# Kernel tuning notes

Hardware: AMD Instinct MI355X
Metric: run time of the kernel (lower is better)

Reference implementation:

```python
import jax, jax.numpy as jnp
import numpy as np

GROUPS = 32
EPS = 1e-5

def setup_inputs() -> dict:
    key = jax.random.key(0)
    k1, k2, k3 = jax.random.split(key, 3)
    C = 512
    x = jax.random.normal(k1, (4, C, 64, 64), dtype=jnp.float32)
    gn_weight = jnp.ones((C,), jnp.float32)
    gn_bias = jnp.zeros((C,), jnp.float32)
    qkv_weight = jax.random.normal(k2, (3 * C, C), jnp.float32) * (1.0 / np.sqrt(C))
    proj_weight = jax.random.normal(k3, (C, C), jnp.float32) * (1.0 / np.sqrt(C))
    proj_bias = jnp.zeros((C,), jnp.float32)
    return {"x": x, "gn_weight": gn_weight, "gn_bias": gn_bias,
            "qkv_weight": qkv_weight, "proj_weight": proj_weight, "proj_bias": proj_bias}

def reference(x, gn_weight, gn_bias, qkv_weight, proj_weight, proj_bias):
    n, c, h, w = x.shape
    residue = x
    # GroupNorm(32, c): normalize over (c//32 channels * h * w) per group
    xg = x.reshape(n, GROUPS, -1)
    mu = xg.mean(axis=-1, keepdims=True)
    var = xg.var(axis=-1, keepdims=True)
    xn = (xg - mu) * jax.lax.rsqrt(var + EPS)
    xn = xn.reshape(n, c, h, w) * gn_weight[None, :, None, None] + gn_bias[None, :, None, None]
    # tokens: [n, T, c] with T = h*w
    t = xn.reshape(n, c, h * w).transpose(0, 2, 1)
    # qkv linear (no bias), n_heads = 1 so head_size = c
    qkv = jnp.einsum('ntc,dc->ntd', t, qkv_weight)
    q, k, v = jnp.split(qkv, 3, axis=-1)
    scale = 1.0 / np.sqrt(c)
    scores = jnp.einsum('nqc,nkc->nqk', q, k) * scale  # [n, T, T]
    weights = jax.nn.softmax(scores, axis=-1)
    out = jnp.einsum('nqk,nkc->nqc', weights, v)
    out = jnp.einsum('ntc,dc->ntd', out, proj_weight) + proj_bias
    out = out.transpose(0, 2, 1).reshape(n, c, h, w)
    return out + residue
```

## Files before the change

kernel.cpp:

```cpp
#include <hip/hip_runtime.h>
#include <hip/hip_bf16.h>

typedef __bf16 bf16;
typedef __bf16 bf16x8 __attribute__((ext_vector_type(8)));
typedef float f32x4 __attribute__((ext_vector_type(4)));

__device__ __forceinline__ void gload_lds16(const bf16* g, bf16* l) {
    __builtin_amdgcn_global_load_lds(
        (const __attribute__((address_space(1))) void*)g,
        (__attribute__((address_space(3))) void*)l, 16, 0, 0);
}

__global__ __launch_bounds__(256) void k_gnstats(const float* __restrict__ x,
                                                 float2* __restrict__ stats) {
    const int g = blockIdx.x;
    const float4* p = (const float4*)(x + (long)g * 65536);
    float s = 0.f, ss = 0.f;
    #pragma unroll 8
    for (int i = 0; i < 64; ++i) {
        float4 v = p[threadIdx.x + i * 256];
        s  += v.x + v.y + v.z + v.w;
        ss += v.x * v.x + v.y * v.y + v.z * v.z + v.w * v.w;
    }
    #pragma unroll
    for (int off = 32; off >= 1; off >>= 1) {
        s  += __shfl_down(s, off);
        ss += __shfl_down(ss, off);
    }
    __shared__ float rs[4], rss[4];
    if ((threadIdx.x & 63) == 0) { rs[threadIdx.x >> 6] = s; rss[threadIdx.x >> 6] = ss; }
    __syncthreads();
    if (threadIdx.x == 0) {
        float S  = rs[0] + rs[1] + rs[2] + rs[3];
        float SS = rss[0] + rss[1] + rss[2] + rss[3];
        float mu = S * (1.f / 65536.f);
        float var = SS * (1.f / 65536.f) - mu * mu;
        stats[g] = make_float2(mu, rsqrtf(var + 1e-5f));
    }
}

__global__ __launch_bounds__(256) void k_norm_t(const float* __restrict__ x,
                                                const float* __restrict__ w,
                                                const float* __restrict__ b,
                                                const float2* __restrict__ stats,
                                                bf16* __restrict__ t) {
    __shared__ float tile[64][65];
    const int bid = blockIdx.x;
    const int n = bid >> 9, rem = bid & 511;
    const int s0 = (rem >> 3) * 64, c0 = (rem & 7) * 64;
    const int tid = threadIdx.x;
    const int sl = tid & 63, cq = tid >> 6;
    #pragma unroll
    for (int i = 0; i < 16; ++i) {
        const int cl = cq * 16 + i;
        const int c = c0 + cl;
        const float2 st = stats[n * 32 + (c >> 4)];
        const float v = x[((long)(n * 512 + c)) * 4096 + s0 + sl];
        tile[cl][sl] = (v - st.x) * st.y * w[c] + b[c];
    }
    __syncthreads();
    #pragma unroll
    for (int i = 0; i < 16; ++i) {
        const int sl2 = cq * 16 + i;
        const int cl2 = tid & 63;
        t[((long)(n * 4096 + s0 + sl2)) * 512 + c0 + cl2] = (bf16)tile[cl2][sl2];
    }
}

__global__ __launch_bounds__(256) void k_convw(const float* __restrict__ qw,
                                               const float* __restrict__ pw,
                                               bf16* __restrict__ qwb,
                                               bf16* __restrict__ pwb) {
    const int i = blockIdx.x * 256 + threadIdx.x;
    if (i < 786432) {
        float v = qw[i];
        if (i < 512 * 512) v *= 0.06376281516217733f;
        qwb[i] = (bf16)v;
    } else {
        const int j = i - 786432;
        pwb[j] = (bf16)pw[j];
    }
}

__global__ __launch_bounds__(256) void k_vt(const bf16* __restrict__ vbuf,
                                            bf16* __restrict__ Vt) {
    __shared__ bf16 tile[64][66];
    const int bid = blockIdx.x;
    const int n = bid >> 9, rem = bid & 511;
    const int s0 = (rem >> 3) * 64, d0 = (rem & 7) * 64;
    const int tid = threadIdx.x;
    #pragma unroll
    for (int i = 0; i < 16; ++i) {
        const int sl = (tid >> 6) * 16 + i;
        const int dl = tid & 63;
        tile[sl][dl] = vbuf[((long)(n * 4096 + s0 + sl)) * 512 + d0 + dl];
    }
    __syncthreads();
    #pragma unroll
    for (int i = 0; i < 16; ++i) {
        const int dl = (tid >> 6) * 16 + i;
        const int sl = tid & 63;
        Vt[((long)(n * 512 + d0 + dl)) * 4096 + s0 + sl] = tile[sl][dl];
    }
}

#define PH(mh, kk, S_, WN)                                                         \
  {                                                                                \
    if ((mh) == 0) {                                                               \
      _Pragma("unroll")                                                            \
      for (int n = 0; n < 4; ++n) {                                                \
        int row = wn * 64 + n * 16 + lr;                                           \
        int cg = lg ^ ((row >> 1) & 3);                                            \
        bfr[n] = *(const bf16x8*)(BsT + (kk) * 8192 + row * 32 + cg * 8);          \
      }                                                                            \
    }                                                                              \
    _Pragma("unroll")                                                              \
    for (int i = 0; i < 4; ++i) {                                                  \
      int row = wm * 128 + ((mh) * 4 + i) * 16 + lr;                               \
      int cg = lg ^ ((row >> 1) & 3);                                              \
      af[i] = *(const bf16x8*)(AsT + (kk) * 8192 + row * 32 + cg * 8);             \
    }                                                                              \
    if ((S_) >= 0) issue_unit(S_);                                                 \
    __builtin_amdgcn_s_barrier();                                                  \
    asm volatile("" ::: "memory");                                                 \
    __builtin_amdgcn_s_setprio(1);                                                 \
    _Pragma("unroll")                                                              \
    for (int i = 0; i < 4; ++i)                                                    \
      _Pragma("unroll")                                                            \
      for (int n = 0; n < 4; ++n)                                                  \
        acc[(mh) * 4 + i][n] =                                                     \
            __builtin_amdgcn_mfma_f32_16x16x32_bf16(af[i], bfr[n],                 \
                                                    acc[(mh) * 4 + i][n], 0, 0, 0);\
    __builtin_amdgcn_s_setprio(0);                                                 \
    if constexpr ((WN) >= 0)                                                       \
      asm volatile("s_waitcnt vmcnt(%0)" ::"i"(WN) : "memory");                    \
    __builtin_amdgcn_s_barrier();                                                  \
    asm volatile("" ::: "memory");                                                 \
  }

template <int EPI>
__global__ __launch_bounds__(512, 2) void gemm256(
    const bf16* __restrict__ A, int lda, long aZ,
    const bf16* __restrict__ B, int ldb, long bZ,
    bf16* __restrict__ C, int ldc, long cZ, int K,
    bf16* __restrict__ vbuf) {
    __shared__ bf16 As[2 * 2 * 256 * 32];
    __shared__ bf16 Bs[2 * 2 * 256 * 32];
    const int t = threadIdx.x;
    const int wid = t >> 6, l = t & 63;
    const int wm = wid >> 2, wn = wid & 3;
    const int lr = l & 15;
    const int lg = l >> 4;
    const long z = blockIdx.z;

    const int gx = gridDim.x;
    int nwg = gx * gridDim.y;
    int flat = blockIdx.y * gx + blockIdx.x;
    if ((nwg & 7) == 0) { int qq = nwg >> 3; flat = (flat & 7) * qq + (flat >> 3); }
    const int bx = flat % gx, by = flat / gx;

    const bf16* Ab = A + z * aZ + (long)bx * 256 * lda;
    const bf16* Bb = B + z * bZ + (long)by * 256 * ldb;

    const int NT = K >> 6;
    const int NT4 = NT << 2;

    f32x4 acc[8][4];
    #pragma unroll
    for (int i = 0; i < 8; ++i)
        #pragma unroll
        for (int n = 0; n < 4; ++n) acc[i][n] = f32x4{0.f, 0.f, 0.f, 0.f};

    const int srow = t >> 2;
    const int scg0 = t & 3;

    auto issue_unit = [&](int s) {
        int ti = s >> 2, idx = s & 3;
        int kh = idx >> 1, isB = idx & 1;
        const bf16* g = isB ? Bb : Ab;
        int ld = isB ? ldb : lda;
        bf16* lp = (isB ? Bs : As) + ((ti & 1) * 2 + kh) * 8192;
        int k0 = ti * 64 + kh * 32;
        #pragma unroll
        for (int j = 0; j < 2; ++j) {
            int row = j * 128 + srow;
            int cg = scg0 ^ ((row >> 1) & 3);
            gload_lds16(g + (long)row * ld + k0 + cg * 8, lp + (j * 512 + t) * 8);
        }
    };

    #pragma unroll
    for (int s = 0; s < 6; ++s) issue_unit(s);
    asm volatile("s_waitcnt vmcnt(8)" ::: "memory");
    __builtin_amdgcn_s_barrier();
    asm volatile("" ::: "memory");

    bf16x8 bfr[4], af[4];

    for (int ti = 0; ti < NT - 2; ++ti) {
        const bf16* AsT = As + (ti & 1) * 16384;
        const bf16* BsT = Bs + (ti & 1) * 16384;
        const int sb = 4 * ti + 6;
        PH(0, 0, sb + 0, -1)
        PH(1, 0, sb + 1, 8)
        PH(0, 1, sb + 2, -1)
        PH(1, 1, sb + 3, 8)
    }
    {
        const bf16* AsT = As + ((NT - 2) & 1) * 16384;
        const bf16* BsT = Bs + ((NT - 2) & 1) * 16384;
        PH(0, 0, NT4 - 2, -1)
        PH(1, 0, NT4 - 1, 8)
        PH(0, 1, -1, -1)
        PH(1, 1, -1, 4)
    }
    {
        const bf16* AsT = As + ((NT - 1) & 1) * 16384;
        const bf16* BsT = Bs + ((NT - 1) & 1) * 16384;
        PH(0, 0, -1, -1)
        PH(1, 0, -1, 0)
        PH(0, 1, -1, -1)
        PH(1, 1, -1, -1)
    }

    const int row0 = bx * 256 + wm * 128;
    const int col0 = by * 256 + wn * 64;
    const int rq = lg * 4;

    if (EPI == 1) {
        bf16* Cz = C + z * cZ;
        #pragma unroll
        for (int i = 0; i < 8; ++i)
            #pragma unroll
            for (int n = 0; n < 4; ++n) {
                const int col = col0 + n * 16 + lr;
                #pragma unroll
                for (int r = 0; r < 4; ++r)
                    Cz[(long)(row0 + i * 16 + rq + r) * ldc + col] = (bf16)exp2f(acc[i][n][r]);
            }
    } else {
        #pragma unroll
        for (int i = 0; i < 8; ++i) {
            const int row = row0 + i * 16 + rq;
            #pragma unroll
            for (int n = 0; n < 4; ++n) {
                const int col = col0 + n * 16 + lr;
                if (col < 1024) {
                    #pragma unroll
                    for (int r = 0; r < 4; ++r)
                        C[(long)(row + r) * 1024 + col] = (bf16)acc[i][n][r];
                } else {
                    #pragma unroll
                    for (int r = 0; r < 4; ++r)
                        vbuf[(long)(row + r) * 512 + (col - 1024)] = (bf16)acc[i][n][r];
                }
            }
        }
    }
}

__global__ __launch_bounds__(512, 1) void k_pv(
    const bf16* __restrict__ P, const bf16* __restrict__ Vt,
    bf16* __restrict__ O, int ldo) {
    __shared__ bf16 Bs[2][512 * 64];
    __shared__ bf16 As[2][64 * 64];
    __shared__ float linv[64];
    const int t = threadIdx.x;
    const int w = t >> 6, l = t & 63, lr = l & 15, lg = l >> 4;
    const int lr7 = lr & 7;
    const int sr = t >> 3, sc8 = t & 7, sr7 = sr & 7;
    const long zz = blockIdx.y;
    const int bx = blockIdx.x;

    const bf16* Pg = P + zz * ((long)4096 * 4096) + (long)(bx * 64 + sr) * 4096 + (sc8 ^ sr7) * 8;
    const bf16* Vg = Vt + zz * ((long)512 * 4096) + (long)sr * 4096 + (sc8 ^ sr7) * 8;

    auto issue = [&](int tile, int buf) {
        gload_lds16(Pg + tile * 64, As[buf] + t * 8);
        #pragma unroll
        for (int u = 0; u < 8; ++u)
            gload_lds16(Vg + (long)u * 64 * 4096 + tile * 64, Bs[buf] + u * 4096 + t * 8);
    };

    f32x4 acc[4][4];
    #pragma unroll
    for (int i = 0; i < 4; ++i)
        #pragma unroll
        for (int n = 0; n < 4; ++n) acc[i][n] = f32x4{0.f, 0.f, 0.f, 0.f};

    float lsum = 0.f;

    issue(0, 0);
    issue(1, 1);

    for (int ti = 0; ti < 64; ++ti) {
        if (ti < 63) { asm volatile("s_waitcnt vmcnt(9)" ::: "memory"); }
        else         { asm volatile("s_waitcnt vmcnt(0)" ::: "memory"); }
        __builtin_amdgcn_s_barrier();
        asm volatile("" ::: "memory");

        const bf16* Asb = As[ti & 1];
        const bf16* Bsb = Bs[ti & 1];

        {
            bf16x8 sv = *(const bf16x8*)(Asb + t * 8);
            #pragma unroll
            for (int j = 0; j < 8; ++j) lsum += (float)sv[j];
        }

        __builtin_amdgcn_s_setprio(1);
        #pragma unroll
        for (int kk = 0; kk < 2; ++kk) {
            bf16x8 af[4], bfv[4];
            #pragma unroll
            for (int mi = 0; mi < 4; ++mi)
                af[mi] = *(const bf16x8*)(Asb + (mi * 16 + lr) * 64 + (((kk * 4 + lg) ^ lr7) * 8));
            #pragma unroll
            for (int n = 0; n < 4; ++n)
                bfv[n] = *(const bf16x8*)(Bsb + (w * 64 + n * 16 + lr) * 64 + (((kk * 4 + lg) ^ lr7) * 8));
            #pragma unroll
            for (int mi = 0; mi < 4; ++mi)
                #pragma unroll
                for (int n = 0; n < 4; ++n)
                    acc[mi][n] = __builtin_amdgcn_mfma_f32_16x16x32_bf16(af[mi], bfv[n], acc[mi][n], 0, 0, 0);
        }
        __builtin_amdgcn_s_setprio(0);

        __builtin_amdgcn_s_barrier();
        asm volatile("" ::: "memory");
        if (ti < 62) issue(ti + 2, ti & 1);
    }

    lsum += __shfl_xor(lsum, 1);
    lsum += __shfl_xor(lsum, 2);
    lsum += __shfl_xor(lsum, 4);
    if (sc8 == 0) linv[sr] = 1.f / lsum;
    asm volatile("s_waitcnt lgkmcnt(0)" ::: "memory");
    __builtin_amdgcn_s_barrier();
    asm volatile("" ::: "memory");

    bf16* Oz = O + zz * ((long)4096 * ldo);
    #pragma unroll
    for (int mi = 0; mi < 4; ++mi) {
        float4 lv = *(const float4*)&linv[mi * 16 + lg * 4];
        #pragma unroll
        for (int n = 0; n < 4; ++n) {
            const long base = (long)(bx * 64 + mi * 16 + lg * 4) * ldo + w * 64 + n * 16 + lr;
            Oz[base]           = (bf16)(acc[mi][n][0] * lv.x);
            Oz[base + ldo]     = (bf16)(acc[mi][n][1] * lv.y);
            Oz[base + 2 * ldo] = (bf16)(acc[mi][n][2] * lv.z);
            Oz[base + 3 * ldo] = (bf16)(acc[mi][n][3] * lv.w);
        }
    }
}

#define PH128(nh, kk, S_, WN)                                                      \
  {                                                                                \
    if ((nh) == 0) {                                                               \
      _Pragma("unroll")                                                            \
      for (int i = 0; i < 4; ++i) {                                                \
        int row = wm * 64 + i * 16 + lr;                                           \
        int cg = lg ^ ((row >> 1) & 3);                                            \
        af[i] = *(const bf16x8*)(AsT + (kk) * 8192 + row * 32 + cg * 8);           \
      }                                                                            \
    }                                                                              \
    _Pragma("unroll")                                                              \
    for (int j = 0; j < 2; ++j) {                                                  \
      int row = wn * 64 + ((nh) * 2 + j) * 16 + lr;                                \
      int cg = lg ^ ((row >> 1) & 3);                                              \
      bfr[j] = *(const bf16x8*)(BsT + (kk) * 4096 + row * 32 + cg * 8);            \
    }                                                                              \
    if ((S_) >= 0) issue_unit(S_);                                                 \
    __builtin_amdgcn_s_barrier();                                                  \
    asm volatile("" ::: "memory");                                                 \
    __builtin_amdgcn_s_setprio(1);                                                 \
    _Pragma("unroll")                                                              \
    for (int i = 0; i < 4; ++i)                                                    \
      _Pragma("unroll")                                                            \
      for (int j = 0; j < 2; ++j)                                                  \
        acc[i][(nh) * 2 + j] =                                                     \
            __builtin_amdgcn_mfma_f32_16x16x32_bf16(af[i], bfr[j],                 \
                                                    acc[i][(nh) * 2 + j], 0, 0, 0);\
    __builtin_amdgcn_s_setprio(0);                                                 \
    if constexpr ((WN) >= 0)                                                       \
      asm volatile("s_waitcnt vmcnt(%0)" ::"i"(WN) : "memory");                    \
    __builtin_amdgcn_s_barrier();                                                  \
    asm volatile("" ::: "memory");                                                 \
  }

__global__ __launch_bounds__(512, 2) void gemm_proj(
    const bf16* __restrict__ A, int lda,
    const bf16* __restrict__ B, int ldb,
    const float* __restrict__ bias,
    float* __restrict__ Cout) {
    __shared__ bf16 As[2 * 2 * 256 * 32];
    __shared__ bf16 Bs[2 * 2 * 128 * 32];
    const int t = threadIdx.x;
    const int wid = t >> 6, l = t & 63;
    const int wm = wid >> 1, wn = wid & 1;
    const int lr = l & 15;
    const int lg = l >> 4;

    const int gx = gridDim.x;
    int nwg = gx * gridDim.y;
    int flat = blockIdx.y * gx + blockIdx.x;
    if ((nwg & 7) == 0) { int qq = nwg >> 3; flat = (flat & 7) * qq + (flat >> 3); }
    const int bx = flat % gx, by = flat / gx;

    const bf16* Ab = A + (long)bx * 256 * lda;
    const bf16* Bb = B + (long)by * 128 * ldb;

    const int NT = 8;
    const int NT4 = 32;

    f32x4 acc[4][4];
    #pragma unroll
    for (int i = 0; i < 4; ++i)
        #pragma unroll
        for (int n = 0; n < 4; ++n) acc[i][n] = f32x4{0.f, 0.f, 0.f, 0.f};

    const int srow = t >> 2;
    const int scg0 = t & 3;

    auto issue_unit = [&](int s) {
        int ti = s >> 2, idx = s & 3;
        int kh = idx >> 1, isB = idx & 1;
        int k0 = ti * 64 + kh * 32;
        if (isB) {
            bf16* lp = Bs + ((ti & 1) * 2 + kh) * 4096;
            int cg = scg0 ^ ((srow >> 1) & 3);
            gload_lds16(Bb + (long)srow * ldb + k0 + cg * 8, lp + t * 8);
        } else {
            bf16* lp = As + ((ti & 1) * 2 + kh) * 8192;
            #pragma unroll
            for (int j = 0; j < 2; ++j) {
                int row = j * 128 + srow;
                int cg = scg0 ^ ((row >> 1) & 3);
                gload_lds16(Ab + (long)row * lda + k0 + cg * 8, lp + (j * 512 + t) * 8);
            }
        }
    };

    #pragma unroll
    for (int s = 0; s < 6; ++s) issue_unit(s);
    asm volatile("s_waitcnt vmcnt(6)" ::: "memory");
    __builtin_amdgcn_s_barrier();
    asm volatile("" ::: "memory");

    bf16x8 bfr[2], af[4];

    for (int ti = 0; ti < NT - 2; ++ti) {
        const bf16* AsT = As + (ti & 1) * 16384;
        const bf16* BsT = Bs + (ti & 1) * 8192;
        const int sb = 4 * ti + 6;
        PH128(0, 0, sb + 0, -1)
        PH128(1, 0, sb + 1, 6)
        PH128(0, 1, sb + 2, -1)
        PH128(1, 1, sb + 3, 6)
    }
    {
        const bf16* AsT = As + ((NT - 2) & 1) * 16384;
        const bf16* BsT = Bs + ((NT - 2) & 1) * 8192;
        PH128(0, 0, NT4 - 2, -1)
        PH128(1, 0, NT4 - 1, 6)
        PH128(0, 1, -1, -1)
        PH128(1, 1, -1, 3)
    }
    {
        const bf16* AsT = As + ((NT - 1) & 1) * 16384;
        const bf16* BsT = Bs + ((NT - 1) & 1) * 8192;
        PH128(0, 0, -1, -1)
        PH128(1, 0, -1, 0)
        PH128(0, 1, -1, -1)
        PH128(1, 1, -1, -1)
    }

    const int row0 = bx * 256 + wm * 64;
    const int col0 = by * 128 + wn * 64;
    const int rq = lg * 4;
    #pragma unroll
    for (int i = 0; i < 4; ++i)
        #pragma unroll
        for (int n = 0; n < 4; ++n) {
            const int col = col0 + n * 16 + lr;
            #pragma unroll
            for (int r = 0; r < 4; ++r)
                Cout[(long)(row0 + i * 16 + rq + r) * 512 + col] = acc[i][n][r] + bias[col];
        }
}

__global__ __launch_bounds__(256) void k_final(const float* __restrict__ pb,
                                               const float* __restrict__ x,
                                               float* __restrict__ out) {
    __shared__ float tile[64][65];
    const int bid = blockIdx.x;
    const int n = bid >> 9, rem = bid & 511;
    const int s0 = (rem >> 3) * 64, c0 = (rem & 7) * 64;
    const int tid = threadIdx.x;
    #pragma unroll
    for (int i = 0; i < 16; ++i) {
        const int sl = (tid >> 6) * 16 + i;
        const int cl = tid & 63;
        tile[sl][cl] = pb[((long)(n * 4096 + s0 + sl)) * 512 + c0 + cl];
    }
    __syncthreads();
    #pragma unroll
    for (int i = 0; i < 16; ++i) {
        const int cl = (tid >> 6) * 16 + i;
        const int sl = tid & 63;
        const long oi = ((long)(n * 512 + c0 + cl)) * 4096 + s0 + sl;
        out[oi] = tile[sl][cl] + x[oi];
    }
}

extern "C" void kernel_launch(void* const* d_in, const int* in_sizes, int n_in,
                              void* d_out, int out_size, void* d_ws, size_t ws_size,
                              hipStream_t stream) {
    const float* x     = (const float*)d_in[0];
    const float* gnw   = (const float*)d_in[1];
    const float* gnb   = (const float*)d_in[2];
    const float* qkvw  = (const float*)d_in[3];
    const float* projw = (const float*)d_in[4];
    const float* projb = (const float*)d_in[5];

    char* ws = (char*)d_ws;
    size_t off = 0;
    auto alloc = [&](size_t bytes) {
        void* p = ws + off;
        off += (bytes + 255) & ~(size_t)255;
        return p;
    };
    bf16*   qwb   = (bf16*)alloc((size_t)1536 * 512 * 2);
    bf16*   pwb   = (bf16*)alloc((size_t)512 * 512 * 2);
    float2* stats = (float2*)alloc((size_t)128 * 8);
    bf16*   qk    = (bf16*)alloc((size_t)16384 * 1024 * 2);
    bf16*   Vt    = (bf16*)alloc((size_t)4 * 512 * 4096 * 2);
    char*   R     = (char*)alloc((size_t)4 * 4096 * 4096 * 2);
    bf16*   tbuf  = (bf16*)R;
    bf16*   vbuf  = (bf16*)(R + (size_t)16384 * 512 * 2);
    bf16*   Sbuf  = (bf16*)R;
    float*  pjout = (float*)R;

    k_gnstats<<<128, 256, 0, stream>>>(x, stats);
    k_norm_t<<<2048, 256, 0, stream>>>(x, gnw, gnb, stats, tbuf);
    k_convw<<<4096, 256, 0, stream>>>(qkvw, projw, qwb, pwb);

    gemm256<2><<<dim3(64, 6, 1), 512, 0, stream>>>(
        tbuf, 512, 0, qwb, 512, 0, qk, 1024, 0, 512, vbuf);

    k_vt<<<2048, 256, 0, stream>>>(vbuf, Vt);

    const long QZ = (long)4096 * 1024;
    const long SZ = (long)4096 * 4096;
    gemm256<1><<<dim3(16, 16, 4), 512, 0, stream>>>(
        qk, 1024, QZ,
        qk + 512, 1024, QZ,
        Sbuf, 4096, SZ, 512, nullptr);
    k_pv<<<dim3(64, 4), 512, 0, stream>>>(Sbuf, Vt, qk, 1024);

    gemm_proj<<<dim3(64, 4), 512, 0, stream>>>(
        qk, 1024, pwb, 512, projb, pjout);

    k_final<<<2048, 256, 0, stream>>>(pjout, x, (float*)d_out);
}
```

Before: 304.6 us.

## Halve PV k-tile to fit two blocks per CU and remap blocks to XCDs

The P·V kernel now uses a K-tile of 32 instead of 64, halving LDS use so two 512-thread blocks can share a CU (launch bounds raised to 2). The LDS swizzle and load mapping are rewritten for 32-wide rows. The block index is remapped so each XCD handles a contiguous batch of rows of one batch element, which should improve L2 reuse of Vt. The trade-offs are twice as many barrier iterations with less MFMA work per sync, and tighter register limits from the occupancy bound.

```diff
diff --git a/kernel.cpp b/kernel.cpp
--- a/kernel.cpp
+++ b/kernel.cpp
@@ -259,27 +259,39 @@
     }
 }
 
-__global__ __launch_bounds__(512, 1) void k_pv(
+__global__ __launch_bounds__(512, 2) void k_pv(
     const bf16* __restrict__ P, const bf16* __restrict__ Vt,
     bf16* __restrict__ O, int ldo) {
-    __shared__ bf16 Bs[2][512 * 64];
-    __shared__ bf16 As[2][64 * 64];
+    __shared__ bf16 Bs[2][512 * 32];
+    __shared__ bf16 As[2][64 * 32];
     __shared__ float linv[64];
     const int t = threadIdx.x;
     const int w = t >> 6, l = t & 63, lr = l & 15, lg = l >> 4;
-    const int lr7 = lr & 7;
-    const int sr = t >> 3, sc8 = t & 7, sr7 = sr & 7;
-    const long zz = blockIdx.y;
-    const int bx = blockIdx.x;
-
-    const bf16* Pg = P + zz * ((long)4096 * 4096) + (long)(bx * 64 + sr) * 4096 + (sc8 ^ sr7) * 8;
-    const bf16* Vg = Vt + zz * ((long)512 * 4096) + (long)sr * 4096 + (sc8 ^ sr7) * 8;
-
-    auto issue = [&](int tile, int buf) {
-        gload_lds16(Pg + tile * 64, As[buf] + t * 8);
-        #pragma unroll
-        for (int u = 0; u < 8; ++u)
-            gload_lds16(Vg + (long)u * 64 * 4096 + tile * 64, Bs[buf] + u * 4096 + t * 8);
+    const int cgr = lg ^ ((lr >> 1) & 3);
+
+    int f = blockIdx.y * 64 + blockIdx.x;
+    const int xcd = f & 7, idx = f >> 3;
+    const long zz = xcd >> 1;
+    const int bx = (xcd & 1) * 32 + idx;
+
+    const int vr = t >> 2;
+    const int vg = (t & 3) ^ ((vr >> 1) & 3);
+    const bf16* Vgp = Vt + zz * ((long)512 * 4096) + (long)vr * 4096 + vg * 8;
+    const int q = w & 3;
+    const int prl = l >> 2;
+    const int pg = (l & 3) ^ ((l >> 3) & 3);
+    const bf16* Pgp = P + zz * ((long)4096 * 4096)
+                        + (long)(bx * 64 + q * 16 + prl) * 4096 + pg * 8;
+
+    bf16* Asl = &As[0][0];
+    bf16* Bsl = &Bs[0][0];
+
+    auto issue = [&](int ti, int buf) {
+        gload_lds16(Pgp + ti * 32, Asl + buf * 2048 + q * 512 + l * 8);
+        #pragma unroll
+        for (int u = 0; u < 4; ++u)
+            gload_lds16(Vgp + (long)u * 128 * 4096 + ti * 32,
+                        Bsl + buf * 16384 + u * 4096 + t * 8);
     };
 
     f32x4 acc[4][4];
@@ -293,48 +305,46 @@
     issue(0, 0);
     issue(1, 1);
 
-    for (int ti = 0; ti < 64; ++ti) {
-        if (ti < 63) { asm volatile("s_waitcnt vmcnt(9)" ::: "memory"); }
-        else         { asm volatile("s_waitcnt vmcnt(0)" ::: "memory"); }
+    for (int ti = 0; ti < 128; ++ti) {
+        if (ti < 127) { asm volatile("s_waitcnt vmcnt(5)" ::: "memory"); }
+        else          { asm volatile("s_waitcnt vmcnt(0)" ::: "memory"); }
         __builtin_amdgcn_s_barrier();
         asm volatile("" ::: "memory");
 
-        const bf16* Asb = As[ti & 1];
-        const bf16* Bsb = Bs[ti & 1];
-
-        {
-            bf16x8 sv = *(const bf16x8*)(Asb + t * 8);
+        const bf16* Asb = Asl + (ti & 1) * 2048;
+        const bf16* Bsb = Bsl + (ti & 1) * 16384;
+
+        if (w < 4) {
+            bf16x8 sv = *(const bf16x8*)(Asb + q * 512 + l * 8);
             #pragma unroll
             for (int j = 0; j < 8; ++j) lsum += (float)sv[j];
         }
 
         __builtin_amdgcn_s_setprio(1);
-        #pragma unroll
-        for (int kk = 0; kk < 2; ++kk) {
-            bf16x8 af[4], bfv[4];
-            #pragma unroll
-            for (int mi = 0; mi < 4; ++mi)
-                af[mi] = *(const bf16x8*)(Asb + (mi * 16 + lr) * 64 + (((kk * 4 + lg) ^ lr7) * 8));
+        bf16x8 af[4], bfv[4];
+        #pragma unroll
+        for (int mi = 0; mi < 4; ++mi)
+            af[mi] = *(const bf16x8*)(Asb + (mi * 16 + lr) * 32 + cgr * 8);
+        #pragma unroll
+        for (int n = 0; n < 4; ++n)
+            bfv[n] = *(const bf16x8*)(Bsb + (w * 64 + n * 16 + lr) * 32 + cgr * 8);
+        #pragma unroll
+        for (int mi = 0; mi < 4; ++mi)
             #pragma unroll
             for (int n = 0; n < 4; ++n)
-                bfv[n] = *(const bf16x8*)(Bsb + (w * 64 + n * 16 + lr) * 64 + (((kk * 4 + lg) ^ lr7) * 8));
-            #pragma unroll
-            for (int mi = 0; mi < 4; ++mi)
-                #pragma unroll
-                for (int n = 0; n < 4; ++n)
-                    acc[mi][n] = __builtin_amdgcn_mfma_f32_16x16x32_bf16(af[mi], bfv[n], acc[mi][n], 0, 0, 0);
-        }
+                acc[mi][n] = __builtin_amdgcn_mfma_f32_16x16x32_bf16(af[mi], bfv[n], acc[mi][n], 0, 0, 0);
         __builtin_amdgcn_s_setprio(0);
 
         __builtin_amdgcn_s_barrier();
         asm volatile("" ::: "memory");
-        if (ti < 62) issue(ti + 2, ti & 1);
-    }
-
-    lsum += __shfl_xor(lsum, 1);
-    lsum += __shfl_xor(lsum, 2);
-    lsum += __shfl_xor(lsum, 4);
-    if (sc8 == 0) linv[sr] = 1.f / lsum;
+        if (ti < 126) issue(ti + 2, ti & 1);
+    }
+
+    if (w < 4) {
+        lsum += __shfl_xor(lsum, 1);
+        lsum += __shfl_xor(lsum, 2);
+        if ((l & 3) == 0) linv[q * 16 + prl] = 1.f / lsum;
+    }
     asm volatile("s_waitcnt lgkmcnt(0)" ::: "memory");
     __builtin_amdgcn_s_barrier();
     asm volatile("" ::: "memory");
```

New measurement: 335.3 us. 1.1x slower.

## Make GEMM blocks persistent over multiple output tiles with continuous prefetch

Applied to the files above, without the earlier changes.

The templated GEMM now makes each workgroup compute several output tiles in sequence: two column tiles for the QKV projection, and all four batch slices for the QK^T score GEMM. The global-to-LDS prefetch pipeline runs across tile boundaries, so the next tile's loads overlap the current tile's epilogue stores. This is meant to remove pipeline fill and drain per tile and cut launch wave count. In exchange the grids are half or a quarter as large, which can leave compute units idle on a 256-CU device, and the outer loop is no longer unrolled.

```diff
diff --git a/kernel.cpp b/kernel.cpp
--- a/kernel.cpp
+++ b/kernel.cpp
@@ -138,11 +138,11 @@
     asm volatile("" ::: "memory");                                                 \
   }
 
-template <int EPI>
-__global__ __launch_bounds__(512, 2) void gemm256(
-    const bf16* __restrict__ A, int lda, long aZ,
-    const bf16* __restrict__ B, int ldb, long bZ,
-    bf16* __restrict__ C, int ldc, long cZ, int K,
+template <int NTILES, int EPI>
+__global__ __launch_bounds__(512, 2) void gemm256p(
+    const bf16* __restrict__ A, int lda, long dA,
+    const bf16* __restrict__ B, int ldb, long dB,
+    bf16* __restrict__ C, int ldc, long dC,
     bf16* __restrict__ vbuf) {
     __shared__ bf16 As[2 * 2 * 256 * 32];
     __shared__ bf16 Bs[2 * 2 * 256 * 32];
@@ -151,7 +151,6 @@
     const int wm = wid >> 2, wn = wid & 3;
     const int lr = l & 15;
     const int lg = l >> 4;
-    const long z = blockIdx.z;
 
     const int gx = gridDim.x;
     int nwg = gx * gridDim.y;
@@ -159,11 +158,10 @@
     if ((nwg & 7) == 0) { int qq = nwg >> 3; flat = (flat & 7) * qq + (flat >> 3); }
     const int bx = flat % gx, by = flat / gx;
 
-    const bf16* Ab = A + z * aZ + (long)bx * 256 * lda;
-    const bf16* Bb = B + z * bZ + (long)by * 256 * ldb;
-
-    const int NT = K >> 6;
-    const int NT4 = NT << 2;
+    const long bxoff = (long)bx * 256 * lda;
+    const long byoff = (long)by * 256 * ldb;
+
+    constexpr int GT = NTILES * 8;
 
     f32x4 acc[8][4];
     #pragma unroll
@@ -175,18 +173,60 @@
     const int scg0 = t & 3;
 
     auto issue_unit = [&](int s) {
-        int ti = s >> 2, idx = s & 3;
+        int tig = s >> 2, idx = s & 3;
+        int j = tig >> 3, til = tig & 7;
         int kh = idx >> 1, isB = idx & 1;
-        const bf16* g = isB ? Bb : Ab;
+        const bf16* g = isB ? (B + (long)j * dB + byoff) : (A + (long)j * dA + bxoff);
         int ld = isB ? ldb : lda;
-        bf16* lp = (isB ? Bs : As) + ((ti & 1) * 2 + kh) * 8192;
-        int k0 = ti * 64 + kh * 32;
-        #pragma unroll
-        for (int j = 0; j < 2; ++j) {
-            int row = j * 128 + srow;
+        bf16* lp = (isB ? Bs : As) + ((tig & 1) * 2 + kh) * 8192;
+        int k0 = til * 64 + kh * 32;
+        #pragma unroll
+        for (int jj = 0; jj < 2; ++jj) {
+            int row = jj * 128 + srow;
             int cg = scg0 ^ ((row >> 1) & 3);
-            gload_lds16(g + (long)row * ld + k0 + cg * 8, lp + (j * 512 + t) * 8);
-        }
+            gload_lds16(g + (long)row * ld + k0 + cg * 8, lp + (jj * 512 + t) * 8);
+        }
+    };
+
+    auto store_tile = [&](int j) {
+        const int row0 = bx * 256 + wm * 128;
+        const int rq = lg * 4;
+        if constexpr (EPI == 1) {
+            bf16* Cz = C + (long)j * dC;
+            const int col0 = by * 256 + wn * 64;
+            #pragma unroll
+            for (int i = 0; i < 8; ++i)
+                #pragma unroll
+                for (int n = 0; n < 4; ++n) {
+                    const int col = col0 + n * 16 + lr;
+                    #pragma unroll
+                    for (int r = 0; r < 4; ++r)
+                        Cz[(long)(row0 + i * 16 + rq + r) * ldc + col] = (bf16)exp2f(acc[i][n][r]);
+                }
+        } else {
+            const int col0 = j * 768 + by * 256 + wn * 64;
+            #pragma unroll
+            for (int i = 0; i < 8; ++i) {
+                const int row = row0 + i * 16 + rq;
+                #pragma unroll
+                for (int n = 0; n < 4; ++n) {
+                    const int col = col0 + n * 16 + lr;
+                    if (col < 1024) {
+                        #pragma unroll
+                        for (int r = 0; r < 4; ++r)
+                            C[(long)(row + r) * 1024 + col] = (bf16)acc[i][n][r];
+                    } else {
+                        #pragma unroll
+                        for (int r = 0; r < 4; ++r)
+                            vbuf[(long)(row + r) * 512 + (col - 1024)] = (bf16)acc[i][n][r];
+                    }
+                }
+            }
+        }
+        #pragma unroll
+        for (int i = 0; i < 8; ++i)
+            #pragma unroll
+            for (int n = 0; n < 4; ++n) acc[i][n] = f32x4{0.f, 0.f, 0.f, 0.f};
     };
 
     #pragma unroll
@@ -197,66 +237,34 @@
 
     bf16x8 bfr[4], af[4];
 
-    for (int ti = 0; ti < NT - 2; ++ti) {
-        const bf16* AsT = As + (ti & 1) * 16384;
-        const bf16* BsT = Bs + (ti & 1) * 16384;
-        const int sb = 4 * ti + 6;
+    #pragma unroll 1
+    for (int gt = 0; gt < GT - 2; ++gt) {
+        const bf16* AsT = As + (gt & 1) * 16384;
+        const bf16* BsT = Bs + (gt & 1) * 16384;
+        const int sb = 4 * gt + 6;
         PH(0, 0, sb + 0, -1)
         PH(1, 0, sb + 1, 8)
         PH(0, 1, sb + 2, -1)
         PH(1, 1, sb + 3, 8)
+        if (NTILES > 1 && (gt & 7) == 7) store_tile(gt >> 3);
     }
     {
-        const bf16* AsT = As + ((NT - 2) & 1) * 16384;
-        const bf16* BsT = Bs + ((NT - 2) & 1) * 16384;
-        PH(0, 0, NT4 - 2, -1)
-        PH(1, 0, NT4 - 1, 8)
+        const bf16* AsT = As + ((GT - 2) & 1) * 16384;
+        const bf16* BsT = Bs + ((GT - 2) & 1) * 16384;
+        PH(0, 0, 4 * GT - 2, -1)
+        PH(1, 0, 4 * GT - 1, 8)
         PH(0, 1, -1, -1)
         PH(1, 1, -1, 4)
     }
     {
-        const bf16* AsT = As + ((NT - 1) & 1) * 16384;
-        const bf16* BsT = Bs + ((NT - 1) & 1) * 16384;
+        const bf16* AsT = As + ((GT - 1) & 1) * 16384;
+        const bf16* BsT = Bs + ((GT - 1) & 1) * 16384;
         PH(0, 0, -1, -1)
         PH(1, 0, -1, 0)
         PH(0, 1, -1, -1)
         PH(1, 1, -1, -1)
     }
-
-    const int row0 = bx * 256 + wm * 128;
-    const int col0 = by * 256 + wn * 64;
-    const int rq = lg * 4;
-
-    if (EPI == 1) {
-        bf16* Cz = C + z * cZ;
-        #pragma unroll
-        for (int i = 0; i < 8; ++i)
-            #pragma unroll
-            for (int n = 0; n < 4; ++n) {
-                const int col = col0 + n * 16 + lr;
-                #pragma unroll
-                for (int r = 0; r < 4; ++r)
-                    Cz[(long)(row0 + i * 16 + rq + r) * ldc + col] = (bf16)exp2f(acc[i][n][r]);
-            }
-    } else {
-        #pragma unroll
-        for (int i = 0; i < 8; ++i) {
-            const int row = row0 + i * 16 + rq;
-            #pragma unroll
-            for (int n = 0; n < 4; ++n) {
-                const int col = col0 + n * 16 + lr;
-                if (col < 1024) {
-                    #pragma unroll
-                    for (int r = 0; r < 4; ++r)
-                        C[(long)(row + r) * 1024 + col] = (bf16)acc[i][n][r];
-                } else {
-                    #pragma unroll
-                    for (int r = 0; r < 4; ++r)
-                        vbuf[(long)(row + r) * 512 + (col - 1024)] = (bf16)acc[i][n][r];
-                }
-            }
-        }
-    }
+    store_tile(NTILES - 1);
 }
 
 __global__ __launch_bounds__(512, 1) void k_pv(
@@ -545,17 +553,17 @@
     k_norm_t<<<2048, 256, 0, stream>>>(x, gnw, gnb, stats, tbuf);
     k_convw<<<4096, 256, 0, stream>>>(qkvw, projw, qwb, pwb);
 
-    gemm256<2><<<dim3(64, 6, 1), 512, 0, stream>>>(
-        tbuf, 512, 0, qwb, 512, 0, qk, 1024, 0, 512, vbuf);
+    gemm256p<2, 2><<<dim3(64, 3), 512, 0, stream>>>(
+        tbuf, 512, 0, qwb, 512, (long)768 * 512, qk, 1024, 0, vbuf);
 
     k_vt<<<2048, 256, 0, stream>>>(vbuf, Vt);
 
     const long QZ = (long)4096 * 1024;
     const long SZ = (long)4096 * 4096;
-    gemm256<1><<<dim3(16, 16, 4), 512, 0, stream>>>(
+    gemm256p<4, 1><<<dim3(16, 16), 512, 0, stream>>>(
         qk, 1024, QZ,
         qk + 512, 1024, QZ,
-        Sbuf, 4096, SZ, 512, nullptr);
+        Sbuf, 4096, SZ, nullptr);
     k_pv<<<dim3(64, 4), 512, 0, stream>>>(Sbuf, Vt, qk, 1024);
 
     gemm_proj<<<dim3(64, 4), 512, 0, stream>>>(
```

After: 321.1 us. +5.4%, slower.
